# Kernel tuning notes

Hardware: AMD Instinct MI355X
Metric: run time of the kernel (lower is better)

Reference implementation:

```python
import jax, jax.numpy as jnp
import numpy as np

BS, T, Q, HID, PROJ = 16, 16, 100, 256, 256


def setup_inputs() -> dict:
    key = jax.random.key(0)
    k1, k2, k3, k4, k5 = jax.random.split(key, 5)
    frame_embeds = jax.random.normal(k1, (BS, T, Q, HID), jnp.float32)
    other_frame_embeds = jax.random.normal(k2, (BS, T, Q, HID), jnp.float32)
    W = jax.random.normal(k3, (HID, PROJ), jnp.float32) / np.sqrt(HID).astype(np.float32)
    b = jax.random.normal(k4, (PROJ,), jnp.float32) * 0.01
    n = BS * Q
    mid = jax.random.randint(k5, (n, 1), 1, T - 1, dtype=jnp.int32)
    bridge = jnp.concatenate(
        [jnp.zeros((n, 1), jnp.int32), mid, jnp.full((n, 1), T - 1, jnp.int32)], axis=1
    )  # (n,3): head=0, random pivot in [1,T-2], tail=T-1
    return {"frame_embeds": frame_embeds, "other_frame_embeds": other_frame_embeds,
            "W": W, "b": b, "bridge": bridge}


def _prep(fe, W, b):
    # Linear proj, (bs,t,q,c)->(bs*q, t, c), L2-normalize per embedding.
    bs, t, q, _ = fe.shape
    x = fe @ W + b
    x = x.transpose(0, 2, 1, 3).reshape(bs * q, t, -1)
    return x / jnp.linalg.norm(x, axis=-1, keepdims=True)


def _forward(frame_embeds, other_frame_embeds, W, b, bridge, delta=0.3):
    cur = _prep(frame_embeds, W, b)      # (n,t,c)
    other = _prep(other_frame_embeds, W, b)
    bh = bridge[:, 0].astype(jnp.float32)
    bp_f = bridge[:, 1].astype(jnp.float32)
    bt = bridge[:, 2].astype(jnp.float32)
    alpha = (bp_f - bh) / (bt - bh)      # (n,)
    sigma = alpha * (bt - bp_f)          # (n,)
    g = jnp.take_along_axis(cur, bridge[:, :, None], axis=1)  # (n,3,c) head/pivot/tail
    # positive brownian-bridge distance
    x = g[:, 1] - (1.0 - alpha)[:, None] * g[:, 0] - alpha[:, None] * g[:, 2]
    numer = jnp.exp(-jnp.sum(x * x, axis=-1) / (2.0 * sigma ** 2))  # (n,)
    # negatives: pivot frame taken from every sequence in [cur; other].
    # ||m_ij - a_i||^2 = ||m_ij||^2 - 2 m_ij.a_i + ||a_i||^2 with m_ij = neg_all[j, bp_i],
    # avoiding the (n,N,3,c) repeat tensor of the original.
    neg_all = jnp.concatenate([cur, other], axis=0)            # (N,t,c)
    a = (1.0 - alpha)[:, None] * g[:, 0] + alpha[:, None] * g[:, 2]  # (n,c)
    cross = jnp.einsum('ic,jtc->ijt', a, neg_all)              # (n,N,t)
    bp = bridge[:, 1]
    cross_g = jnp.take_along_axis(cross, bp[:, None, None], axis=2)[..., 0]  # (n,N)
    nn2_g = jnp.sum(neg_all * neg_all, axis=-1).T[bp]          # (n,N)
    x2 = nn2_g - 2.0 * cross_g + jnp.sum(a * a, axis=-1)[:, None]
    dist = -x2 / (2.0 * sigma ** 2)[:, None]                   # (n,N)
    n = dist.shape[0]
    idx = jnp.arange(n)
    self_dist = dist[idx, idx]
    dist = dist.at[idx, idx].set(-10000.0)
    topv, _ = jax.lax.top_k(dist, 5)
    deno = jnp.exp(jnp.concatenate([self_dist[:, None], topv], axis=-1))  # (n,6)
    brownian_loss = (numer / deno.sum(axis=-1)).mean()
    score = jnp.einsum('nc,nc->n', cur[:, 0], cur[:, -1])
    head_tail_match = jax.nn.softplus(delta - score).mean()
    return brownian_loss, head_tail_match


def reference(frame_embeds, other_frame_embeds, W, b, bridge):
    return _forward(frame_embeds, other_frame_embeds, W, b, bridge)
```

## Files before the change

kernel.cpp:

```cpp
#include <hip/hip_runtime.h>
#include <hip/hip_bf16.h>

#define NROW 1600
#define NEG  3200
#define ROWS_FLAT 25600
#define NSPLIT 25

using bf16x8 = __attribute__((ext_vector_type(8))) short;
using f32x4  = __attribute__((ext_vector_type(4))) float;

__device__ __forceinline__ float bf2f(unsigned v) { return __uint_as_float(v << 16); }
__device__ __forceinline__ ushort f2bf(float f) {
  __hip_bfloat16 h = __float2bfloat16(f);
  return *(ushort*)&h;
}
__device__ __forceinline__ float load1(const ushort* p, size_t idx, int f32) {
  return f32 ? ((const float*)p)[idx] : bf2f(p[idx]);
}
__device__ __forceinline__ void load8(const ushort* p, size_t idx, int f32, float* o) {
  if (f32) {
    const float* q = (const float*)p;
    float4 a = *(const float4*)(q + idx);
    float4 b = *(const float4*)(q + idx + 4);
    o[0]=a.x; o[1]=a.y; o[2]=a.z; o[3]=a.w;
    o[4]=b.x; o[5]=b.y; o[6]=b.z; o[7]=b.w;
  } else {
    uint4 u = *(const uint4*)(p + idx);
    o[0]=bf2f(u.x & 0xffffu); o[1]=bf2f(u.x >> 16);
    o[2]=bf2f(u.y & 0xffffu); o[3]=bf2f(u.y >> 16);
    o[4]=bf2f(u.z & 0xffffu); o[5]=bf2f(u.z >> 16);
    o[6]=bf2f(u.w & 0xffffu); o[7]=bf2f(u.w >> 16);
  }
}
__device__ __forceinline__ int sniff_f32(const ushort* p, int lane) {
  unsigned e = ((unsigned)p[2*lane] >> 7) & 0xffu;
  unsigned long long b = __ballot(e >= 100u && e <= 140u);
  return (__popcll(b) >= 40) ? 0 : 1;
}

__global__ __launch_bounds__(256) void k_prepw(const ushort* __restrict__ W,
    ushort* __restrict__ Wt) {
  int fW = sniff_f32(W, threadIdx.x & 63);
  int n = blockIdx.x, k = threadIdx.x;
  Wt[n*256 + k] = f2bf(load1(W, (size_t)k*256 + n, fW));
}

__global__ __launch_bounds__(256) void k_proj(const ushort* __restrict__ fe0,
    const ushort* __restrict__ fe1, const ushort* __restrict__ Wt,
    const ushort* __restrict__ bias, ushort* __restrict__ Pb) {
  __shared__ union {
    ushort x[64*256];
    ushort c[4][32*72];
  } sh;
  __shared__ float s_ss[4][64];
  const int tid = threadIdx.x;
  const int w = tid >> 6, lane = tid & 63, q = lane >> 4, m = lane & 15;
  const int grow0 = blockIdx.x * 64;
  const int src1 = (grow0 >= ROWS_FLAT);
  const ushort* src = src1 ? fe1 : fe0;
  const size_t rbase = (size_t)(src1 ? grow0 - ROWS_FLAT : grow0) * 256;
  const int fSrc = sniff_f32(src, lane);
  const int fB   = sniff_f32(bias, lane);
  if (!fSrc) {
    #pragma unroll
    for (int i = 0; i < 8; i++) {
      int l = tid + i*256;
      int r = l >> 5, kc = l & 31;
      uint4 u = *(const uint4*)(src + rbase + (size_t)r*256 + kc*8);
      *(uint4*)&sh.x[r*256 + ((kc*8) ^ ((r&7)<<3))] = u;
    }
  } else {
    #pragma unroll
    for (int i = 0; i < 8; i++) {
      int l = tid + i*256;
      int r = l >> 5, kc = l & 31;
      float o[8];
      load8(src, rbase + (size_t)r*256 + kc*8, 1, o);
      uint4 u;
      u.x = (unsigned)f2bf(o[0]) | ((unsigned)f2bf(o[1]) << 16);
      u.y = (unsigned)f2bf(o[2]) | ((unsigned)f2bf(o[3]) << 16);
      u.z = (unsigned)f2bf(o[4]) | ((unsigned)f2bf(o[5]) << 16);
      u.w = (unsigned)f2bf(o[6]) | ((unsigned)f2bf(o[7]) << 16);
      *(uint4*)&sh.x[r*256 + ((kc*8) ^ ((r&7)<<3))] = u;
    }
  }
  __syncthreads();
  f32x4 acc[4][4];
  #pragma unroll
  for (int nt = 0; nt < 4; nt++) {
    float bb = load1(bias, w*64 + nt*16 + m, fB);
    f32x4 v = {bb, bb, bb, bb};
    #pragma unroll
    for (int mt = 0; mt < 4; mt++) acc[mt][nt] = v;
  }
  const int sw = (m & 7) << 3;
  for (int k0 = 0; k0 < 256; k0 += 32) {
    int pk = (k0 + q*8) ^ sw;
    bf16x8 a[4];
    #pragma unroll
    for (int mt = 0; mt < 4; mt++) a[mt] = *(const bf16x8*)&sh.x[(mt*16 + m)*256 + pk];
    #pragma unroll
    for (int nt = 0; nt < 4; nt++) {
      bf16x8 b = *(const bf16x8*)(Wt + (size_t)(w*64 + nt*16 + m)*256 + k0 + q*8);
      #pragma unroll
      for (int mt = 0; mt < 4; mt++)
        acc[mt][nt] = __builtin_amdgcn_mfma_f32_16x16x32_bf16(a[mt], b, acc[mt][nt], 0, 0, 0);
    }
  }
  float ssp[4][4];
  #pragma unroll
  for (int mt = 0; mt < 4; mt++)
    #pragma unroll
    for (int reg = 0; reg < 4; reg++) {
      float s = 0.f;
      #pragma unroll
      for (int nt = 0; nt < 4; nt++) { float v = acc[mt][nt][reg]; s += v*v; }
      ssp[mt][reg] = s;
    }
  #pragma unroll
  for (int mk = 1; mk < 16; mk <<= 1)
    #pragma unroll
    for (int mt = 0; mt < 4; mt++)
      #pragma unroll
      for (int reg = 0; reg < 4; reg++) ssp[mt][reg] += __shfl_xor(ssp[mt][reg], mk, 64);
  if (m == 0)
    #pragma unroll
    for (int mt = 0; mt < 4; mt++)
      #pragma unroll
      for (int reg = 0; reg < 4; reg++) s_ss[w][mt*16 + 4*q + reg] = ssp[mt][reg];
  __syncthreads();
  float inv[4][4];
  #pragma unroll
  for (int mt = 0; mt < 4; mt++)
    #pragma unroll
    for (int reg = 0; reg < 4; reg++) {
      int row = mt*16 + 4*q + reg;
      float s = s_ss[0][row] + s_ss[1][row] + s_ss[2][row] + s_ss[3][row];
      inv[mt][reg] = 1.0f / sqrtf(s);
    }
  #pragma unroll
  for (int half = 0; half < 2; half++) {
    #pragma unroll
    for (int mt = half*2; mt < half*2 + 2; mt++)
      #pragma unroll
      for (int reg = 0; reg < 4; reg++) {
        int rl = (mt - half*2)*16 + 4*q + reg;
        #pragma unroll
        for (int nt = 0; nt < 4; nt++)
          sh.c[w][rl*72 + nt*16 + m] = f2bf(acc[mt][nt][reg] * inv[mt][reg]);
      }
    int rl = (lane >> 3), c16 = lane & 7;
    #pragma unroll
    for (int it = 0; it < 4; it++) {
      int row = it*8 + rl;
      int grow = grow0 + half*32 + row;
      int srcid = grow / ROWS_FLAT;
      int rem   = grow % ROWS_FLAT;
      int b  = rem / 1600;
      int t  = (rem / 100) & 15;
      int qq = rem % 100;
      size_t orow = ((size_t)(srcid*1600 + b*100 + qq) * 16 + t) * 256;
      uint4 v = *(uint4*)&sh.c[w][row*72 + c16*8];
      *(uint4*)(Pb + orow + w*64 + c16*8) = v;
    }
  }
}

__global__ __launch_bounds__(256) void k_bridge(const ushort* __restrict__ Pb,
    const int* __restrict__ bridge, ushort* __restrict__ Ab,
    float* __restrict__ prm, float* __restrict__ numer,
    int* __restrict__ cnt, int* __restrict__ lst, float* __restrict__ wsum) {
  int i = blockIdx.x, c = threadIdx.x;
  int bh = bridge[i*3+0], bp = bridge[i*3+1], bt = bridge[i*3+2];
  float bhf = (float)bh, bpf = (float)bp, btf = (float)bt;
  float alpha = (bpf - bhf) / (btf - bhf);
  float sigma = alpha * (btf - bpf);
  const ushort* base = Pb + (size_t)i * 16 * 256;
  float g0 = bf2f(base[bh*256 + c]), g1 = bf2f(base[bp*256 + c]), g2 = bf2f(base[bt*256 + c]);
  float head = bf2f(base[c]), tail = bf2f(base[15*256 + c]);
  float a = (1.0f - alpha) * g0 + alpha * g2;
  float x = g1 - a;
  Ab[(size_t)i*256 + c] = f2bf(a);
  float xx = x*x, aac = a*a, sc = head*tail;
  #pragma unroll
  for (int mk = 1; mk < 64; mk <<= 1) {
    xx  += __shfl_xor(xx, mk, 64);
    aac += __shfl_xor(aac, mk, 64);
    sc  += __shfl_xor(sc, mk, 64);
  }
  __shared__ float red[3][4];
  int wv = c >> 6;
  if ((c & 63) == 0) { red[0][wv]=xx; red[1][wv]=aac; red[2][wv]=sc; }
  __syncthreads();
  if (c == 0) {
    float XX = red[0][0]+red[0][1]+red[0][2]+red[0][3];
    float AA = red[1][0]+red[1][1]+red[1][2]+red[1][3];
    float SC = red[2][0]+red[2][1]+red[2][2]+red[2][3];
    float inv2s2 = 1.0f / (2.0f * sigma * sigma);
    prm[i*2+0] = inv2s2;
    prm[i*2+1] = AA;
    numer[i] = expf(-XX * inv2s2);
    float sp = log1pf(expf(0.3f - SC));
    atomicAdd(wsum + 1, sp * (1.0f / 1600.0f));
    int pos = atomicAdd(cnt + bp, 1);
    lst[bp * 1600 + pos] = i;
  }
}

__device__ __forceinline__ void sort5(float* c) {
  #define CE(i,j) { float hi = fmaxf(c[i], c[j]), lo = fminf(c[i], c[j]); c[i]=hi; c[j]=lo; }
  CE(0,1) CE(3,4) CE(2,4) CE(2,3) CE(1,4) CE(0,3) CE(0,2) CE(1,3) CE(1,2)
  #undef CE
}
__device__ __forceinline__ void ins5(float* t, float v) {
  float hi, lo;
  hi = fmaxf(t[0], v); lo = fminf(t[0], v); t[0] = hi; v = lo;
  hi = fmaxf(t[1], v); lo = fminf(t[1], v); t[1] = hi; v = lo;
  hi = fmaxf(t[2], v); lo = fminf(t[2], v); t[2] = hi; v = lo;
  hi = fmaxf(t[3], v); lo = fminf(t[3], v); t[3] = hi; v = lo;
  t[4] = fmaxf(t[4], v);
}

__global__ __launch_bounds__(256) void k_cross(const ushort* __restrict__ Pb,
    const ushort* __restrict__ Ab, const float* __restrict__ prm,
    const int* __restrict__ cnt, const int* __restrict__ lst,
    float* __restrict__ part) {
  int t = blockIdx.z;
  int n_t = min(cnt[t], 1600);
  int i0 = blockIdx.y * 32;
  if (i0 >= n_t) return;
  int j0 = blockIdx.x * 128;
  __shared__ int s_gis[32];
  __shared__ float s_red[4][32][6];
  int tid = threadIdx.x;
  if (tid < 32) {
    int gi = lst[t*1600 + min(i0 + tid, n_t - 1)];
    s_gis[tid] = min(max(gi, 0), NROW - 1);
  }
  __syncthreads();
  const int w = tid >> 6, lane = tid & 63, q = lane >> 4, m = lane & 15;
  const ushort* jp0 = Pb + ((size_t)(j0 + w*32 + m)*16 + t) * 256;
  const ushort* jp1 = jp0 + (size_t)16*16*256;
  int gi0 = s_gis[m], gi1 = s_gis[16 + m];
  const ushort* ip0 = Ab + (size_t)gi0 * 256;
  const ushort* ip1 = Ab + (size_t)gi1 * 256;
  f32x4 acc[2][2];
  #pragma unroll
  for (int jt = 0; jt < 2; jt++)
    #pragma unroll
    for (int it = 0; it < 2; it++) { f32x4 z = {0.f,0.f,0.f,0.f}; acc[jt][it] = z; }
  for (int k0 = 0; k0 < 256; k0 += 32) {
    bf16x8 jf0 = *(const bf16x8*)(jp0 + k0 + q*8);
    bf16x8 jf1 = *(const bf16x8*)(jp1 + k0 + q*8);
    bf16x8 if0 = *(const bf16x8*)(ip0 + k0 + q*8);
    bf16x8 if1 = *(const bf16x8*)(ip1 + k0 + q*8);
    acc[0][0] = __builtin_amdgcn_mfma_f32_16x16x32_bf16(jf0, if0, acc[0][0], 0, 0, 0);
    acc[0][1] = __builtin_amdgcn_mfma_f32_16x16x32_bf16(jf0, if1, acc[0][1], 0, 0, 0);
    acc[1][0] = __builtin_amdgcn_mfma_f32_16x16x32_bf16(jf1, if0, acc[1][0], 0, 0, 0);
    acc[1][1] = __builtin_amdgcn_mfma_f32_16x16x32_bf16(jf1, if1, acc[1][1], 0, 0, 0);
  }
  float top[2][5], selfv[2] = {-1e30f, -1e30f};
  float p0i = prm[gi0*2], p0a = prm[gi0*2+1];
  float p1i = prm[gi1*2], p1a = prm[gi1*2+1];
  #pragma unroll
  for (int it = 0; it < 2; it++)
    #pragma unroll
    for (int k = 0; k < 5; k++) top[it][k] = -1e30f;
  #pragma unroll
  for (int jt = 0; jt < 2; jt++)
    #pragma unroll
    for (int reg = 0; reg < 4; reg++) {
      int j = j0 + w*32 + jt*16 + 4*q + reg;
      float d0 = -(1.0f - 2.0f*acc[jt][0][reg] + p0a) * p0i;
      float d1 = -(1.0f - 2.0f*acc[jt][1][reg] + p1a) * p1i;
      if (j == gi0) selfv[0] = d0; else ins5(top[0], d0);
      if (j == gi1) selfv[1] = d1; else ins5(top[1], d1);
    }
  #pragma unroll
  for (int mk = 16; mk <= 32; mk <<= 1) {
    #pragma unroll
    for (int it = 0; it < 2; it++) {
      float o[5], c[5];
      #pragma unroll
      for (int k = 0; k < 5; k++) o[k] = __shfl_xor(top[it][k], mk, 64);
      #pragma unroll
      for (int k = 0; k < 5; k++) c[k] = fmaxf(top[it][k], o[4 - k]);
      sort5(c);
      #pragma unroll
      for (int k = 0; k < 5; k++) top[it][k] = c[k];
      selfv[it] = fmaxf(selfv[it], __shfl_xor(selfv[it], mk, 64));
    }
  }
  if (q == 0) {
    #pragma unroll
    for (int it = 0; it < 2; it++) {
      #pragma unroll
      for (int k = 0; k < 5; k++) s_red[w][it*16 + m][k] = top[it][k];
      s_red[w][it*16 + m][5] = selfv[it];
    }
  }
  __syncthreads();
  if (tid < 32 && i0 + tid < n_t) {
    float T[5], S = s_red[0][tid][5];
    #pragma unroll
    for (int k = 0; k < 5; k++) T[k] = s_red[0][tid][k];
    #pragma unroll
    for (int w2 = 1; w2 < 4; w2++) {
      #pragma unroll
      for (int k = 0; k < 5; k++) ins5(T, s_red[w2][tid][k]);
      S = fmaxf(S, s_red[w2][tid][5]);
    }
    float* pp = part + ((size_t)s_gis[tid]*NSPLIT + blockIdx.x) * 6;
    #pragma unroll
    for (int k = 0; k < 5; k++) pp[k] = T[k];
    pp[5] = S;
  }
}

__global__ __launch_bounds__(64) void k_merge(const float* __restrict__ part,
    const float* __restrict__ numer, float* __restrict__ wsum) {
  int i = blockIdx.x * 64 + threadIdx.x;
  const float* pp = part + (size_t)i * NSPLIT * 6;
  float T[5]; float S = pp[5];
  #pragma unroll
  for (int k = 0; k < 5; k++) T[k] = pp[k];
  #pragma unroll
  for (int s = 1; s < NSPLIT; s++) {
    const float* ps = pp + s*6;
    float v0 = ps[0], v1 = ps[1], v2 = ps[2], v3 = ps[3], v4 = ps[4], v5 = ps[5];
    ins5(T, v0); ins5(T, v1); ins5(T, v2); ins5(T, v3); ins5(T, v4);
    S = fmaxf(S, v5);
  }
  float deno = expf(S);
  #pragma unroll
  for (int k = 0; k < 5; k++) deno += expf(T[k]);
  float local = numer[i] / deno;
  #pragma unroll
  for (int mk = 1; mk < 64; mk <<= 1) local += __shfl_xor(local, mk, 64);
  if (threadIdx.x == 0) atomicAdd(wsum + 0, local * (1.0f / 1600.0f));
}

__global__ void k_out(const float* __restrict__ wsum, const ushort* __restrict__ fe0,
                      void* __restrict__ out) {
  int lane = threadIdx.x & 63;
  int f = sniff_f32(fe0, lane);
  if (lane == 0) {
    if (f) {
      ((float*)out)[0] = wsum[0];
      ((float*)out)[1] = wsum[1];
    } else {
      ushort* o = (ushort*)out;
      o[0] = f2bf(wsum[0]);
      o[1] = f2bf(wsum[1]);
    }
  }
}

extern "C" void kernel_launch(void* const* d_in, const int* in_sizes, int n_in,
                              void* d_out, int out_size, void* d_ws, size_t ws_size,
                              hipStream_t stream) {
  const ushort* fe0    = (const ushort*)d_in[0];
  const ushort* fe1    = (const ushort*)d_in[1];
  const ushort* W      = (const ushort*)d_in[2];
  const ushort* bias   = (const ushort*)d_in[3];
  const int*    bridge = (const int*)d_in[4];

  ushort* Pb    = (ushort*)d_ws;
  ushort* Ab    = Pb + 13107200;
  ushort* Wt    = Ab + 409600;
  float*  part  = (float*)(Wt + 65536);
  float*  prm   = part + 240000;
  float*  numer = prm + 3200;
  float*  wsum  = numer + 1600;
  int*    cnt   = (int*)(wsum + 4);
  int*    lst   = cnt + 16;

  hipMemsetAsync(wsum, 0, 4*sizeof(float) + 16*sizeof(int), stream);

  k_prepw <<<256, 256, 0, stream>>>(W, Wt);
  k_proj  <<<800, 256, 0, stream>>>(fe0, fe1, Wt, bias, Pb);
  k_bridge<<<1600, 256, 0, stream>>>(Pb, bridge, Ab, prm, numer, cnt, lst, wsum);
  k_cross <<<dim3(NSPLIT, 13, 16), 256, 0, stream>>>(Pb, Ab, prm, cnt, lst, part);
  k_merge <<<25, 64, 0, stream>>>(part, numer, wsum);
  k_out   <<<1, 64, 0, stream>>>(wsum, fe0, d_out);
}
```

Baseline: 193.7 us.

## Fold memset and output kernel into other kernels; software-prefetch MFMA operands

Removes the hipMemsetAsync by zeroing the accumulators and counters inside k_prepw, and removes k_out by having the last k_merge block (detected with an atomic counter) write the final output. The MFMA loops in k_proj and k_cross are unrolled and double-buffered so the next k-slice's operands load while the current slice's MFMAs issue. This cuts two launches and aims to hide load latency, at the cost of more registers and reliance on cross-block atomic ordering.

```diff
diff --git a/kernel.cpp b/kernel.cpp
--- a/kernel.cpp
+++ b/kernel.cpp
@@ -39,7 +39,8 @@
 }
 
 __global__ __launch_bounds__(256) void k_prepw(const ushort* __restrict__ W,
-    ushort* __restrict__ Wt) {
+    ushort* __restrict__ Wt, int* __restrict__ zbase) {
+  if (blockIdx.x == 0 && threadIdx.x < 21) zbase[threadIdx.x] = 0;
   int fW = sniff_f32(W, threadIdx.x & 63);
   int n = blockIdx.x, k = threadIdx.x;
   Wt[n*256 + k] = f2bf(load1(W, (size_t)k*256 + n, fW));
@@ -94,17 +95,35 @@
     for (int mt = 0; mt < 4; mt++) acc[mt][nt] = v;
   }
   const int sw = (m & 7) << 3;
-  for (int k0 = 0; k0 < 256; k0 += 32) {
-    int pk = (k0 + q*8) ^ sw;
-    bf16x8 a[4];
-    #pragma unroll
-    for (int mt = 0; mt < 4; mt++) a[mt] = *(const bf16x8*)&sh.x[(mt*16 + m)*256 + pk];
-    #pragma unroll
-    for (int nt = 0; nt < 4; nt++) {
-      bf16x8 b = *(const bf16x8*)(Wt + (size_t)(w*64 + nt*16 + m)*256 + k0 + q*8);
+  const ushort* wbase = Wt + (size_t)(w*64 + m)*256 + q*8;
+  bf16x8 a_cur[4], b_cur[4];
+  #pragma unroll
+  for (int mt = 0; mt < 4; mt++)
+    a_cur[mt] = *(const bf16x8*)&sh.x[(mt*16 + m)*256 + ((q*8) ^ sw)];
+  #pragma unroll
+  for (int nt = 0; nt < 4; nt++)
+    b_cur[nt] = *(const bf16x8*)(wbase + (size_t)nt*16*256);
+  #pragma unroll
+  for (int k = 0; k < 8; k++) {
+    bf16x8 a_nxt[4], b_nxt[4];
+    if (k < 7) {
+      int k0 = (k + 1) * 32;
+      #pragma unroll
+      for (int nt = 0; nt < 4; nt++)
+        b_nxt[nt] = *(const bf16x8*)(wbase + (size_t)nt*16*256 + k0);
+      int pk = (k0 + q*8) ^ sw;
       #pragma unroll
       for (int mt = 0; mt < 4; mt++)
-        acc[mt][nt] = __builtin_amdgcn_mfma_f32_16x16x32_bf16(a[mt], b, acc[mt][nt], 0, 0, 0);
+        a_nxt[mt] = *(const bf16x8*)&sh.x[(mt*16 + m)*256 + pk];
+    }
+    #pragma unroll
+    for (int nt = 0; nt < 4; nt++)
+      #pragma unroll
+      for (int mt = 0; mt < 4; mt++)
+        acc[mt][nt] = __builtin_amdgcn_mfma_f32_16x16x32_bf16(a_cur[mt], b_cur[nt], acc[mt][nt], 0, 0, 0);
+    if (k < 7) {
+      #pragma unroll
+      for (int x = 0; x < 4; x++) { a_cur[x] = a_nxt[x]; b_cur[x] = b_nxt[x]; }
     }
   }
   float ssp[4][4];
@@ -239,25 +258,35 @@
   }
   __syncthreads();
   const int w = tid >> 6, lane = tid & 63, q = lane >> 4, m = lane & 15;
-  const ushort* jp0 = Pb + ((size_t)(j0 + w*32 + m)*16 + t) * 256;
+  const ushort* jp0 = Pb + ((size_t)(j0 + w*32 + m)*16 + t) * 256 + q*8;
   const ushort* jp1 = jp0 + (size_t)16*16*256;
   int gi0 = s_gis[m], gi1 = s_gis[16 + m];
-  const ushort* ip0 = Ab + (size_t)gi0 * 256;
-  const ushort* ip1 = Ab + (size_t)gi1 * 256;
+  const ushort* ip0 = Ab + (size_t)gi0 * 256 + q*8;
+  const ushort* ip1 = Ab + (size_t)gi1 * 256 + q*8;
   f32x4 acc[2][2];
   #pragma unroll
   for (int jt = 0; jt < 2; jt++)
     #pragma unroll
     for (int it = 0; it < 2; it++) { f32x4 z = {0.f,0.f,0.f,0.f}; acc[jt][it] = z; }
-  for (int k0 = 0; k0 < 256; k0 += 32) {
-    bf16x8 jf0 = *(const bf16x8*)(jp0 + k0 + q*8);
-    bf16x8 jf1 = *(const bf16x8*)(jp1 + k0 + q*8);
-    bf16x8 if0 = *(const bf16x8*)(ip0 + k0 + q*8);
-    bf16x8 if1 = *(const bf16x8*)(ip1 + k0 + q*8);
-    acc[0][0] = __builtin_amdgcn_mfma_f32_16x16x32_bf16(jf0, if0, acc[0][0], 0, 0, 0);
-    acc[0][1] = __builtin_amdgcn_mfma_f32_16x16x32_bf16(jf0, if1, acc[0][1], 0, 0, 0);
-    acc[1][0] = __builtin_amdgcn_mfma_f32_16x16x32_bf16(jf1, if0, acc[1][0], 0, 0, 0);
-    acc[1][1] = __builtin_amdgcn_mfma_f32_16x16x32_bf16(jf1, if1, acc[1][1], 0, 0, 0);
+  bf16x8 jc0 = *(const bf16x8*)(jp0);
+  bf16x8 jc1 = *(const bf16x8*)(jp1);
+  bf16x8 ic0 = *(const bf16x8*)(ip0);
+  bf16x8 ic1 = *(const bf16x8*)(ip1);
+  #pragma unroll
+  for (int k = 0; k < 8; k++) {
+    bf16x8 jn0, jn1, in0, in1;
+    if (k < 7) {
+      int o = (k + 1) * 32;
+      jn0 = *(const bf16x8*)(jp0 + o);
+      jn1 = *(const bf16x8*)(jp1 + o);
+      in0 = *(const bf16x8*)(ip0 + o);
+      in1 = *(const bf16x8*)(ip1 + o);
+    }
+    acc[0][0] = __builtin_amdgcn_mfma_f32_16x16x32_bf16(jc0, ic0, acc[0][0], 0, 0, 0);
+    acc[0][1] = __builtin_amdgcn_mfma_f32_16x16x32_bf16(jc0, ic1, acc[0][1], 0, 0, 0);
+    acc[1][0] = __builtin_amdgcn_mfma_f32_16x16x32_bf16(jc1, ic0, acc[1][0], 0, 0, 0);
+    acc[1][1] = __builtin_amdgcn_mfma_f32_16x16x32_bf16(jc1, ic1, acc[1][1], 0, 0, 0);
+    if (k < 7) { jc0 = jn0; jc1 = jn1; ic0 = in0; ic1 = in1; }
   }
   float top[2][5], selfv[2] = {-1e30f, -1e30f};
   float p0i = prm[gi0*2], p0a = prm[gi0*2+1];
@@ -318,7 +347,8 @@
 }
 
 __global__ __launch_bounds__(64) void k_merge(const float* __restrict__ part,
-    const float* __restrict__ numer, float* __restrict__ wsum) {
+    const float* __restrict__ numer, float* __restrict__ wsum, int* __restrict__ done,
+    const ushort* __restrict__ fe0, void* __restrict__ out) {
   int i = blockIdx.x * 64 + threadIdx.x;
   const float* pp = part + (size_t)i * NSPLIT * 6;
   float T[5]; float S = pp[5];
@@ -337,21 +367,27 @@
   float local = numer[i] / deno;
   #pragma unroll
   for (int mk = 1; mk < 64; mk <<= 1) local += __shfl_xor(local, mk, 64);
-  if (threadIdx.x == 0) atomicAdd(wsum + 0, local * (1.0f / 1600.0f));
-}
-
-__global__ void k_out(const float* __restrict__ wsum, const ushort* __restrict__ fe0,
-                      void* __restrict__ out) {
-  int lane = threadIdx.x & 63;
-  int f = sniff_f32(fe0, lane);
-  if (lane == 0) {
-    if (f) {
-      ((float*)out)[0] = wsum[0];
-      ((float*)out)[1] = wsum[1];
-    } else {
-      ushort* o = (ushort*)out;
-      o[0] = f2bf(wsum[0]);
-      o[1] = f2bf(wsum[1]);
+  __shared__ int s_last;
+  if (threadIdx.x == 0) {
+    atomicAdd(wsum + 0, local * (1.0f / 1600.0f));
+    __threadfence();
+    s_last = (atomicAdd(done, 1) == 24);
+  }
+  __syncthreads();
+  if (s_last) {
+    int f = sniff_f32(fe0, threadIdx.x);
+    if (threadIdx.x == 0) {
+      __threadfence();
+      float brown = __hip_atomic_load(wsum + 0, __ATOMIC_RELAXED, __HIP_MEMORY_SCOPE_AGENT);
+      float sp    = __hip_atomic_load(wsum + 1, __ATOMIC_RELAXED, __HIP_MEMORY_SCOPE_AGENT);
+      if (f) {
+        ((float*)out)[0] = brown;
+        ((float*)out)[1] = sp;
+      } else {
+        ushort* o = (ushort*)out;
+        o[0] = f2bf(brown);
+        o[1] = f2bf(sp);
+      }
     }
   }
 }
@@ -373,14 +409,12 @@
   float*  numer = prm + 3200;
   float*  wsum  = numer + 1600;
   int*    cnt   = (int*)(wsum + 4);
-  int*    lst   = cnt + 16;
-
-  hipMemsetAsync(wsum, 0, 4*sizeof(float) + 16*sizeof(int), stream);
-
-  k_prepw <<<256, 256, 0, stream>>>(W, Wt);
+  int*    done  = cnt + 16;
+  int*    lst   = done + 1;
+
+  k_prepw <<<256, 256, 0, stream>>>(W, Wt, (int*)wsum);
   k_proj  <<<800, 256, 0, stream>>>(fe0, fe1, Wt, bias, Pb);
   k_bridge<<<1600, 256, 0, stream>>>(Pb, bridge, Ab, prm, numer, cnt, lst, wsum);
   k_cross <<<dim3(NSPLIT, 13, 16), 256, 0, stream>>>(Pb, Ab, prm, cnt, lst, part);
-  k_merge <<<25, 64, 0, stream>>>(part, numer, wsum);
-  k_out   <<<1, 64, 0, stream>>>(wsum, fe0, d_out);
-}
+  k_merge <<<25, 64, 0, stream>>>(part, numer, wsum, done, fe0, d_out);
+}
```

Measured after the change: 191.7 us. Within noise of the previous version (-1.0%).
